# Performance work log

Measured on AMD Instinct MI355X. Metric: run time of the kernel, lower is better.

The kernel has to match this reference:

```python
import jax, jax.numpy as jnp
import numpy as np

N_NODES = 50000
N_EDGES = 800000
IN_C, HID_C, OUT_C = 256, 256, 64


def _glorot(key, shape):
    fan_in, fan_out = shape[1], shape[0]
    lim = float(np.sqrt(6.0 / (fan_in + fan_out)))
    return jax.random.uniform(key, shape, jnp.float32, -lim, lim)


def setup_inputs() -> dict:
    key = jax.random.key(0)
    ks = jax.random.split(key, 8)
    x = jax.random.normal(ks[0], (N_NODES, IN_C), jnp.float32)
    edge_index = jax.random.randint(ks[1], (2, N_EDGES), 0, N_NODES, jnp.int64)
    # layer 1: SAGEConv(IN_C -> HID_C): lin_l (agg neighbors, has bias), lin_r (root, no bias)
    W_l1 = _glorot(ks[2], (HID_C, IN_C))
    b1 = jnp.zeros((HID_C,), jnp.float32)
    W_r1 = _glorot(ks[3], (HID_C, IN_C))
    # layer 2: SAGEConv(HID_C -> OUT_C)
    W_l2 = _glorot(ks[4], (OUT_C, HID_C))
    b2 = jnp.zeros((OUT_C,), jnp.float32)
    W_r2 = _glorot(ks[5], (OUT_C, HID_C))
    return {"x": x, "W_l1": W_l1, "b1": b1, "W_r1": W_r1,
            "W_l2": W_l2, "b2": b2, "W_r2": W_r2, "edge_index": edge_index}


def _sage_conv(x, src, dst, W_l, b, W_r, n_nodes):
    # mean aggregation of source-node features into destination nodes
    msg = x[src]                                               # [E, C]
    agg = jax.ops.segment_sum(msg, dst, num_segments=n_nodes)  # [N, C]
    deg = jax.ops.segment_sum(jnp.ones((src.shape[0],), x.dtype), dst,
                              num_segments=n_nodes)            # [N]
    agg = agg / jnp.maximum(deg, 1.0)[:, None]
    # out = lin_l(agg) + lin_r(x); bias only on lin_l (PyG SAGEConv default)
    return agg @ W_l.T + b + x @ W_r.T


def reference(x, W_l1, b1, W_r1, W_l2, b2, W_r2, edge_index):
    src, dst = edge_index[0], edge_index[1]
    n = x.shape[0]
    h = _sage_conv(x, src, dst, W_l1, b1, W_r1, n)
    h = jax.nn.relu(h)  # dropout is identity in eval mode
    out = _sage_conv(h, src, dst, W_l2, b2, W_r2, n)
    return out
```

## Files before the change

### kernel.cpp

```cpp
#include <hip/hip_runtime.h>

#define IN_C 256
#define HID_C 256
#define OUT_C 64

#define NBK 64
#define NPAD 50176
#define N2 (NPAD / 2)
#define NCH (NPAD / 256)

typedef __attribute__((ext_vector_type(8))) short bf16x8;
typedef __attribute__((ext_vector_type(4))) float f32x4;
typedef __attribute__((ext_vector_type(2))) float f32x2;
typedef __attribute__((ext_vector_type(8))) unsigned short ushortx8;
typedef __attribute__((ext_vector_type(4))) unsigned int u32x4;
typedef __attribute__((ext_vector_type(2))) unsigned int u32x2;

__device__ inline float b2f(unsigned short u) {
    union { unsigned int u; float f; } v; v.u = ((unsigned int)u) << 16; return v.f;
}
__device__ inline unsigned short f2b(float f) {
    union { float f; unsigned int u; } v; v.f = f;
    unsigned int u = v.u;
    unsigned int r = (u + 0x7fffu + ((u >> 16) & 1u)) >> 16;
    return (unsigned short)r;
}

__device__ __forceinline__ unsigned char f2fp8(float v) {
    int pk = __builtin_amdgcn_cvt_pk_fp8_f32(v, v, 0, false);
    return (unsigned char)(pk & 0xff);
}
__device__ __forceinline__ void fp8acc4(unsigned int w, float& a0, float& a1, float& a2, float& a3) {
    f32x2 lo = __builtin_amdgcn_cvt_pk_f32_fp8((int)w, false);
    f32x2 hi = __builtin_amdgcn_cvt_pk_f32_fp8((int)w, true);
    a0 += lo.x; a1 += lo.y; a2 += hi.x; a3 += hi.y;
}

__device__ __forceinline__ void gl2lds16(const ushort* g, ushort* l) {
    __builtin_amdgcn_global_load_lds((const __attribute__((address_space(1))) void*)g,
                                     (__attribute__((address_space(3))) void*)l, 16, 0, 0);
}

__device__ __forceinline__ void conv8(const float* __restrict__ src, ushort* __restrict__ dst, int u) {
    const float4* p = (const float4*)(src + (size_t)u * 8);
    float4 a = p[0], b = p[1];
    ushort4 o0 = make_ushort4(f2b(a.x), f2b(a.y), f2b(a.z), f2b(a.w));
    ushort4 o1 = make_ushort4(f2b(b.x), f2b(b.y), f2b(b.z), f2b(b.w));
    ((ushort4*)(dst + (size_t)u * 8))[0] = o0;
    ((ushort4*)(dst + (size_t)u * 8))[1] = o1;
}


__global__ __launch_bounds__(1024) void k_front(const int* __restrict__ dst, int E, int EPB,
                                                ushort* __restrict__ rank,
                                                unsigned int* __restrict__ cnt32,
                                                int* __restrict__ chunkpart,
                                                const float* __restrict__ x, ushort* __restrict__ xb,
                                                int xUnits,
                                                const float* __restrict__ Wl1, const float* __restrict__ Wr1,
                                                const float* __restrict__ Wl2, const float* __restrict__ Wr2,
                                                ushort* __restrict__ Wc1, ushort* __restrict__ Wc2) {
    const int bid = blockIdx.x;
    const int t = threadIdx.x;

    if (bid < NBK) {
        __shared__ unsigned int h[N2];
        for (int i = t; i < N2; i += 1024) h[i] = 0;
        __syncthreads();

        const int e0 = bid * EPB;
        const int e1 = min(e0 + EPB, E);
        for (int e = e0 + t; e < e1; e += 1024) {
            int d = dst[e];
            int sh = (d & 1) << 4;
            unsigned int old = atomicAdd(&h[d >> 1], 1u << sh);
            rank[e] = (ushort)((old >> sh) & 0xffffu);
        }
        __syncthreads();

        unsigned int* outp = cnt32 + (size_t)bid * N2;
        for (int i = t; i < N2; i += 1024) outp[i] = h[i];

        if (t < NCH) {
            int c = t;
            int sum = 0;
#pragma unroll 8
            for (int j = 0; j < 128; ++j) {
                unsigned int v = h[c * 128 + ((j + c) & 127)];
                sum += (int)(v & 0xffffu) + (int)(v >> 16);
            }
            chunkpart[c * NBK + bid] = sum;
        }
        return;
    }

    const int ct = (bid - NBK) * 1024 + t;
    const int cn = 256 * 1024;
    for (int i = ct; i < 20480; i += cn) {
        if (i < 8192)       conv8(Wl1, Wc1,         i);
        else if (i < 16384) conv8(Wr1, Wc1 + 65536, i - 8192);
        else if (i < 18432) conv8(Wl2, Wc2,         i - 16384);
        else                conv8(Wr2, Wc2 + 16384, i - 18432);
    }
    for (int u = ct; u < xUnits; u += cn) conv8(x, xb, u);
}


__global__ __launch_bounds__(256) void k_scan(const unsigned int* __restrict__ cnt32,
                                              const int* __restrict__ chunkpart, int N,
                                              int* __restrict__ row_start,
                                              ushort* __restrict__ off16) {
    __shared__ int s[256];
    const int bid = blockIdx.x;
    const int t = threadIdx.x;

    int pre = 0;
    const int limit = bid * NBK;
    for (int i = t; i < limit; i += 256) pre += chunkpart[i];
    s[t] = pre;
    __syncthreads();
    for (int o = 128; o > 0; o >>= 1) {
        if (t < o) s[t] += s[t + o];
        __syncthreads();
    }
    const int chunk_off = s[0];
    __syncthreads();

    const int i = bid * 256 + t;
    const ushort* cnt16 = (const ushort*)cnt32;
    int run = 0;
#pragma unroll 8
    for (int b = 0; b < NBK; ++b) {
        ushort cv = cnt16[(size_t)b * NPAD + i];
        off16[(size_t)b * NPAD + i] = (ushort)run;
        run += cv;
    }
    int deg = run;

    s[t] = deg;
    __syncthreads();
    for (int o = 1; o < 256; o <<= 1) {
        int xx = (t >= o) ? s[t - o] : 0;
        __syncthreads();
        s[t] += xx;
        __syncthreads();
    }
    if (i < N) row_start[i + 1] = s[t] + chunk_off;
    if (i == 0) row_start[0] = 0;
}


__global__ __launch_bounds__(256) void k_gemm_mfma(const ushort* __restrict__ A,
                                                   const ushort* __restrict__ W,
                                                   unsigned char* __restrict__ Cp,
                                                   ushort* __restrict__ Cr,
                                                   int N, int K, int PC, int nby, int nwg,
                                                   int nScat,
                                                   const int* __restrict__ src, const int* __restrict__ dst,
                                                   const ushort* __restrict__ rank,
                                                   const int* __restrict__ row_start,
                                                   const ushort* __restrict__ off16,
                                                   int E, int EPB, int* __restrict__ eidx) {
    if (blockIdx.x < (unsigned)nScat) {
        int base = blockIdx.x * 256 + threadIdx.x;
        int stride = nScat * 256;
        for (int e = base; e < E; e += stride) {
            int d = dst[e];
            int b = e / EPB;
            eidx[row_start[d] + (int)off16[(size_t)b * NPAD + d] + (int)rank[e]] = src[e];
        }
        return;
    }

    __shared__ ushort As[128 * 64];
    __shared__ ushort Bs[128 * 64];

    const int orig = blockIdx.x - nScat;
    const int q = nwg >> 3, r = nwg & 7;
    const int xcd = orig & 7;
    const int base = (xcd < r) ? xcd * (q + 1) : r * (q + 1) + (xcd - r) * q;
    const int wgid = base + (orig >> 3);
    const int bx = wgid / nby, by = wgid % nby;

    const int wid  = threadIdx.x >> 6;
    const int lane = threadIdx.x & 63;
    const int wr = wid >> 1, wc = wid & 1;
    const int bm = bx * 128;
    const int bn = by * 128;
    const int lr = lane & 15;
    const int lk = lane >> 4;
    const int srow   = lane >> 3;
    const int schunk = lane & 7;

    f32x4 acc[4][4];
#pragma unroll
    for (int m = 0; m < 4; ++m)
#pragma unroll
        for (int n = 0; n < 4; ++n) acc[m][n] = (f32x4){0.f, 0.f, 0.f, 0.f};

    for (int k0 = 0; k0 < K; k0 += 64) {
#pragma unroll
        for (int i = 0; i < 4; ++i) {
            int seg = wid * 4 + i;
            int row = seg * 8 + srow;
            gl2lds16(A + (size_t)(bm + row) * K + k0 + schunk * 8, As + seg * 512);
            gl2lds16(W + (size_t)(bn + row) * K + k0 + schunk * 8, Bs + seg * 512);
        }
        __syncthreads();

#pragma unroll
        for (int ks = 0; ks < 2; ++ks) {
            bf16x8 a[4], b[4];
#pragma unroll
            for (int m = 0; m < 4; ++m)
                a[m] = *(const bf16x8*)(As + (wr * 64 + m * 16 + lr) * 64 + ks * 32 + lk * 8);
#pragma unroll
            for (int n = 0; n < 4; ++n)
                b[n] = *(const bf16x8*)(Bs + (wc * 64 + n * 16 + lr) * 64 + ks * 32 + lk * 8);
#pragma unroll
            for (int m = 0; m < 4; ++m)
#pragma unroll
                for (int n = 0; n < 4; ++n)
                    acc[m][n] = __builtin_amdgcn_mfma_f32_16x16x32_bf16(a[m], b[n], acc[m][n], 0, 0, 0);
        }
        __syncthreads();
    }

    const bool isP = (bn + wc * 64) < PC;
#pragma unroll
    for (int m = 0; m < 4; ++m)
#pragma unroll
        for (int r2 = 0; r2 < 4; ++r2) {
            int row = bm + wr * 64 + m * 16 + lk * 4 + r2;
            if (row < N) {
                if (isP) {
#pragma unroll
                    for (int n = 0; n < 4; ++n) {
                        int col = bn + wc * 64 + n * 16 + lr;
                        Cp[(size_t)row * PC + col] = f2fp8(acc[m][n][r2]);
                    }
                } else {
#pragma unroll
                    for (int n = 0; n < 4; ++n) {
                        int col = bn + wc * 64 + n * 16 + lr - PC;
                        Cr[(size_t)row * PC + col] = f2b(acc[m][n][r2]);
                    }
                }
            }
        }
}


__global__ __launch_bounds__(256) void k_agg1(const unsigned char* __restrict__ P1,
                                              const ushort* __restrict__ R1,
                                              const float* __restrict__ bias,
                                              const int* __restrict__ row_start,
                                              const int* __restrict__ eidx,
                                              ushort* __restrict__ h, int N) {
    int node = (blockIdx.x * blockDim.x + threadIdx.x) >> 6;
    int lane = threadIdx.x & 63;
    if (node >= N) return;
    const int slot = lane >> 4;
    const int sub  = lane & 15;
    int s0 = row_start[node], s1 = row_start[node + 1];

    float acc[16];
#pragma unroll
    for (int i = 0; i < 16; ++i) acc[i] = 0.f;

    for (int e = s0 + slot; e < s1; e += 16) {
        int e1 = e + 4, e2 = e + 8, e3 = e + 12;
        bool h1 = e1 < s1, h2 = e2 < s1, h3 = e3 < s1;
        int sA = eidx[e];
        int sB = h1 ? eidx[e1] : sA;
        int sC = h2 ? eidx[e2] : sA;
        int sD = h3 ? eidx[e3] : sA;
        u32x4 a = *(const u32x4*)(P1 + (size_t)sA * 256 + sub * 16);
        u32x4 b = *(const u32x4*)(P1 + (size_t)sB * 256 + sub * 16);
        u32x4 c = *(const u32x4*)(P1 + (size_t)sC * 256 + sub * 16);
        u32x4 d = *(const u32x4*)(P1 + (size_t)sD * 256 + sub * 16);
#pragma unroll
        for (int w = 0; w < 4; ++w) fp8acc4(a[w], acc[w*4], acc[w*4+1], acc[w*4+2], acc[w*4+3]);
        if (h1) {
#pragma unroll
            for (int w = 0; w < 4; ++w) fp8acc4(b[w], acc[w*4], acc[w*4+1], acc[w*4+2], acc[w*4+3]);
        }
        if (h2) {
#pragma unroll
            for (int w = 0; w < 4; ++w) fp8acc4(c[w], acc[w*4], acc[w*4+1], acc[w*4+2], acc[w*4+3]);
        }
        if (h3) {
#pragma unroll
            for (int w = 0; w < 4; ++w) fp8acc4(d[w], acc[w*4], acc[w*4+1], acc[w*4+2], acc[w*4+3]);
        }
    }

#pragma unroll
    for (int i = 0; i < 16; ++i) {
        acc[i] += __shfl_xor(acc[i], 16, 64);
        acc[i] += __shfl_xor(acc[i], 32, 64);
    }

    if (slot == 0) {
        int d = s1 - s0;
        float inv = 1.0f / (float)(d > 1 ? d : 1);
        const ushort* rp = R1 + (size_t)node * 256 + sub * 16;
        ushortx8 r0 = *(const ushortx8*)(rp);
        ushortx8 r1 = *(const ushortx8*)(rp + 8);
        const float* bp = bias + sub * 16;
        ushortx8 o0, o1;
#pragma unroll
        for (int i = 0; i < 8; ++i) {
            float v0 = fmaxf(acc[i] * inv + bp[i] + b2f(r0[i]), 0.f);
            float v1 = fmaxf(acc[i + 8] * inv + bp[i + 8] + b2f(r1[i]), 0.f);
            o0[i] = f2b(v0);
            o1[i] = f2b(v1);
        }
        ushort* hp = h + (size_t)node * 256 + sub * 16;
        *(ushortx8*)(hp) = o0;
        *(ushortx8*)(hp + 8) = o1;
    }
}


__global__ __launch_bounds__(256) void k_agg2(const unsigned char* __restrict__ P2,
                                              const ushort* __restrict__ R2,
                                              const float* __restrict__ bias,
                                              const int* __restrict__ row_start,
                                              const int* __restrict__ eidx,
                                              float* __restrict__ out, int N) {
    int node = (blockIdx.x * blockDim.x + threadIdx.x) >> 6;
    int lane = threadIdx.x & 63;
    if (node >= N) return;
    const int slot = lane >> 3;
    const int sub  = lane & 7;
    int s0 = row_start[node], s1 = row_start[node + 1];

    float acc[8];
#pragma unroll
    for (int i = 0; i < 8; ++i) acc[i] = 0.f;

    for (int e = s0 + slot; e < s1; e += 32) {
        int e1 = e + 8, e2 = e + 16, e3 = e + 24;
        bool h1 = e1 < s1, h2 = e2 < s1, h3 = e3 < s1;
        int sA = eidx[e];
        int sB = h1 ? eidx[e1] : sA;
        int sC = h2 ? eidx[e2] : sA;
        int sD = h3 ? eidx[e3] : sA;
        u32x2 a = *(const u32x2*)(P2 + (size_t)sA * 64 + sub * 8);
        u32x2 b = *(const u32x2*)(P2 + (size_t)sB * 64 + sub * 8);
        u32x2 c = *(const u32x2*)(P2 + (size_t)sC * 64 + sub * 8);
        u32x2 d = *(const u32x2*)(P2 + (size_t)sD * 64 + sub * 8);
#pragma unroll
        for (int w = 0; w < 2; ++w) fp8acc4(a[w], acc[w*4], acc[w*4+1], acc[w*4+2], acc[w*4+3]);
        if (h1) {
#pragma unroll
            for (int w = 0; w < 2; ++w) fp8acc4(b[w], acc[w*4], acc[w*4+1], acc[w*4+2], acc[w*4+3]);
        }
        if (h2) {
#pragma unroll
            for (int w = 0; w < 2; ++w) fp8acc4(c[w], acc[w*4], acc[w*4+1], acc[w*4+2], acc[w*4+3]);
        }
        if (h3) {
#pragma unroll
            for (int w = 0; w < 2; ++w) fp8acc4(d[w], acc[w*4], acc[w*4+1], acc[w*4+2], acc[w*4+3]);
        }
    }

#pragma unroll
    for (int i = 0; i < 8; ++i) {
        acc[i] += __shfl_xor(acc[i], 8, 64);
        acc[i] += __shfl_xor(acc[i], 16, 64);
        acc[i] += __shfl_xor(acc[i], 32, 64);
    }

    if (slot == 0) {
        int d = s1 - s0;
        float inv = 1.0f / (float)(d > 1 ? d : 1);
        ushortx8 rv = *(const ushortx8*)(R2 + (size_t)node * 64 + sub * 8);
        const float* bp = bias + sub * 8;
        float o[8];
#pragma unroll
        for (int i = 0; i < 8; ++i) o[i] = acc[i] * inv + bp[i] + b2f(rv[i]);
        float4* op = (float4*)(out + (size_t)node * 64 + sub * 8);
        op[0] = make_float4(o[0], o[1], o[2], o[3]);
        op[1] = make_float4(o[4], o[5], o[6], o[7]);
    }
}


extern "C" void kernel_launch(void* const* d_in, const int* in_sizes, int n_in,
                              void* d_out, int out_size, void* d_ws, size_t ws_size,
                              hipStream_t stream) {
    const float* x    = (const float*)d_in[0];
    const float* W_l1 = (const float*)d_in[1];
    const float* b1   = (const float*)d_in[2];
    const float* W_r1 = (const float*)d_in[3];
    const float* W_l2 = (const float*)d_in[4];
    const float* b2   = (const float*)d_in[5];
    const float* W_r2 = (const float*)d_in[6];
    const int*   ei   = (const int*)d_in[7];

    const int N = in_sizes[0] / IN_C;
    const int E = in_sizes[7] / 2;
    const int EPB = (E + NBK - 1) / NBK;
    const int* src = ei;
    const int* dst = ei + E;

    char* ws = (char*)d_ws;
    size_t off_ = 0;
    auto alloc = [&](size_t bytes) -> void* {
        void* p = ws + off_;
        off_ += (bytes + 255) & ~(size_t)255;
        return p;
    };
    unsigned int*  cnt32     = (unsigned int*)alloc((size_t)NBK * N2 * 4);
    ushort*        off16     = (ushort*)alloc((size_t)NBK * NPAD * 2);
    int*           chunkpart = (int*)alloc((size_t)NCH * NBK * 4);
    int*           row_start = (int*)alloc((size_t)(N + 1) * 4);
    ushort*        rank      = (ushort*)alloc((size_t)E * 2);
    int*           eidx      = (int*)alloc((size_t)E * 4);
    ushort*        xb        = (ushort*)alloc((size_t)N * IN_C * 2);
    ushort*        Wc1       = (ushort*)alloc((size_t)2 * HID_C * IN_C * 2);
    ushort*        Wc2       = (ushort*)alloc((size_t)2 * OUT_C * HID_C * 2);
    unsigned char* P1        = (unsigned char*)alloc((size_t)N * HID_C);
    ushort*        R1        = (ushort*)alloc((size_t)N * HID_C * 2);
    ushort*        h         = (ushort*)alloc((size_t)N * HID_C * 2);
    unsigned char* P2        = (unsigned char*)alloc((size_t)N * OUT_C);
    ushort*        R2        = (ushort*)alloc((size_t)N * OUT_C * 2);
    (void)alloc(128 * 512 * 2);
    (void)ws_size; (void)n_in; (void)out_size;

    {
        int xUnits = N * IN_C / 8;
        k_front<<<NBK + 256, 1024, 0, stream>>>(dst, E, EPB, rank, cnt32, chunkpart,
                                                x, xb, xUnits,
                                                W_l1, W_r1, W_l2, W_r2, Wc1, Wc2);
    }

    k_scan<<<NCH, 256, 0, stream>>>(cnt32, chunkpart, N, row_start, off16);

    {
        const int nScat = 128;
        int nbx = (N + 127) / 128, nby = (2 * HID_C) / 128;
        int nwg = nbx * nby;
        k_gemm_mfma<<<nScat + nwg, 256, 0, stream>>>(xb, Wc1, P1, R1, N, IN_C, HID_C, nby, nwg,
                                                     nScat, src, dst, rank, row_start, off16,
                                                     E, EPB, eidx);
        k_agg1<<<(N + 3) / 4, 256, 0, stream>>>(P1, R1, b1, row_start, eidx, h, N);
    }

    {
        int nbx = (N + 127) / 128, nby = (2 * OUT_C) / 128;
        int nwg = nbx * nby;
        k_gemm_mfma<<<nwg, 256, 0, stream>>>(h, Wc2, P2, R2, N, HID_C, OUT_C, nby, nwg,
                                             0, nullptr, nullptr, nullptr, nullptr, nullptr,
                                             0, 0, nullptr);
        k_agg2<<<(N + 3) / 4, 256, 0, stream>>>(P2, R2, b2, row_start, eidx, (float*)d_out, N);
    }
}
```

Baseline: 149.3 us.

## Replace LDS-tiled GEMM with register-direct double-buffered MFMA kernels per layer

Drops the shared-memory staged 128x128 GEMM and adds two specialized kernels that load bf16 fragments straight from global memory into registers, double-buffered across K steps. Layer 1 uses 32-row tiles with each wave covering 128 output columns, and layer 2 uses 128-row tiles with a single column block. The edge-scatter blocks now work on contiguous edge ranges, and their count rises from 128 to 448. The aim is to remove LDS traffic and barriers and to raise the block count. The cost is redundant global and L2 reads of the weight rows and A rows, plus higher register pressure.

After: 196.4 us. 1.32x slower.

```diff
diff --git a/kernel.cpp b/kernel.cpp
--- a/kernel.cpp
+++ b/kernel.cpp
@@ -34,11 +34,6 @@
     f32x2 lo = __builtin_amdgcn_cvt_pk_f32_fp8((int)w, false);
     f32x2 hi = __builtin_amdgcn_cvt_pk_f32_fp8((int)w, true);
     a0 += lo.x; a1 += lo.y; a2 += hi.x; a3 += hi.y;
-}
-
-__device__ __forceinline__ void gl2lds16(const ushort* g, ushort* l) {
-    __builtin_amdgcn_global_load_lds((const __attribute__((address_space(1))) void*)g,
-                                     (__attribute__((address_space(3))) void*)l, 16, 0, 0);
 }
 
 __device__ __forceinline__ void conv8(const float* __restrict__ src, ushort* __restrict__ dst, int u) {
@@ -150,101 +145,152 @@
 }
 
 
-__global__ __launch_bounds__(256) void k_gemm_mfma(const ushort* __restrict__ A,
-                                                   const ushort* __restrict__ W,
-                                                   unsigned char* __restrict__ Cp,
-                                                   ushort* __restrict__ Cr,
-                                                   int N, int K, int PC, int nby, int nwg,
-                                                   int nScat,
-                                                   const int* __restrict__ src, const int* __restrict__ dst,
-                                                   const ushort* __restrict__ rank,
-                                                   const int* __restrict__ row_start,
-                                                   const ushort* __restrict__ off16,
-                                                   int E, int EPB, int* __restrict__ eidx) {
+__global__ __launch_bounds__(256) void k_gemm_l1(const ushort* __restrict__ A,
+                                                 const ushort* __restrict__ W,
+                                                 unsigned char* __restrict__ Cp,
+                                                 ushort* __restrict__ Cr,
+                                                 int N, int nScat, int nwg,
+                                                 const int* __restrict__ src, const int* __restrict__ dst,
+                                                 const ushort* __restrict__ rank,
+                                                 const int* __restrict__ row_start,
+                                                 const ushort* __restrict__ off16,
+                                                 int E, int EPB, int per, int* __restrict__ eidx) {
     if (blockIdx.x < (unsigned)nScat) {
-        int base = blockIdx.x * 256 + threadIdx.x;
-        int stride = nScat * 256;
-        for (int e = base; e < E; e += stride) {
+        const int e0 = blockIdx.x * per;
+        const int e1 = min(e0 + per, E);
+        for (int e = e0 + (int)threadIdx.x; e < e1; e += 256) {
             int d = dst[e];
             int b = e / EPB;
             eidx[row_start[d] + (int)off16[(size_t)b * NPAD + d] + (int)rank[e]] = src[e];
         }
         return;
     }
-
-    __shared__ ushort As[128 * 64];
-    __shared__ ushort Bs[128 * 64];
 
     const int orig = blockIdx.x - nScat;
     const int q = nwg >> 3, r = nwg & 7;
     const int xcd = orig & 7;
     const int base = (xcd < r) ? xcd * (q + 1) : r * (q + 1) + (xcd - r) * q;
-    const int wgid = base + (orig >> 3);
-    const int bx = wgid / nby, by = wgid % nby;
-
-    const int wid  = threadIdx.x >> 6;
-    const int lane = threadIdx.x & 63;
-    const int wr = wid >> 1, wc = wid & 1;
-    const int bm = bx * 128;
-    const int bn = by * 128;
-    const int lr = lane & 15;
-    const int lk = lane >> 4;
-    const int srow   = lane >> 3;
-    const int schunk = lane & 7;
-
-    f32x4 acc[4][4];
-#pragma unroll
-    for (int m = 0; m < 4; ++m)
-#pragma unroll
-        for (int n = 0; n < 4; ++n) acc[m][n] = (f32x4){0.f, 0.f, 0.f, 0.f};
-
-    for (int k0 = 0; k0 < K; k0 += 64) {
-#pragma unroll
-        for (int i = 0; i < 4; ++i) {
-            int seg = wid * 4 + i;
-            int row = seg * 8 + srow;
-            gl2lds16(A + (size_t)(bm + row) * K + k0 + schunk * 8, As + seg * 512);
-            gl2lds16(W + (size_t)(bn + row) * K + k0 + schunk * 8, Bs + seg * 512);
-        }
-        __syncthreads();
-
-#pragma unroll
-        for (int ks = 0; ks < 2; ++ks) {
-            bf16x8 a[4], b[4];
-#pragma unroll
-            for (int m = 0; m < 4; ++m)
-                a[m] = *(const bf16x8*)(As + (wr * 64 + m * 16 + lr) * 64 + ks * 32 + lk * 8);
-#pragma unroll
-            for (int n = 0; n < 4; ++n)
-                b[n] = *(const bf16x8*)(Bs + (wc * 64 + n * 16 + lr) * 64 + ks * 32 + lk * 8);
-#pragma unroll
-            for (int m = 0; m < 4; ++m)
-#pragma unroll
-                for (int n = 0; n < 4; ++n)
-                    acc[m][n] = __builtin_amdgcn_mfma_f32_16x16x32_bf16(a[m], b[n], acc[m][n], 0, 0, 0);
-        }
-        __syncthreads();
-    }
-
-    const bool isP = (bn + wc * 64) < PC;
-#pragma unroll
-    for (int m = 0; m < 4; ++m)
+    const int bx = base + (orig >> 3);
+
+    const int t = threadIdx.x;
+    const int wid = t >> 6, lane = t & 63;
+    const int lr = lane & 15, lk = lane >> 4;
+    const int rowb = bx * 32;
+    const int colb = wid * 128;
+
+    const ushort* pa0 = A + (size_t)(rowb + lr) * 256 + lk * 8;
+    const ushort* pa1 = pa0 + 16 * 256;
+    const ushort* pb[8];
+#pragma unroll
+    for (int n = 0; n < 8; ++n) pb[n] = W + (size_t)(colb + n * 16 + lr) * 256 + lk * 8;
+
+    f32x4 acc[2][8];
+#pragma unroll
+    for (int m = 0; m < 2; ++m)
+#pragma unroll
+        for (int n = 0; n < 8; ++n) acc[m][n] = (f32x4){0.f, 0.f, 0.f, 0.f};
+
+    bf16x8 aA[2], bA[8], aB[2], bB[8];
+
+#define LD_AB(av, bv, s)                                                   \
+    {                                                                      \
+        av[0] = *(const bf16x8*)(pa0 + (s) * 32);                          \
+        av[1] = *(const bf16x8*)(pa1 + (s) * 32);                          \
+        _Pragma("unroll")                                                  \
+        for (int n_ = 0; n_ < 8; ++n_)                                     \
+            bv[n_] = *(const bf16x8*)(pb[n_] + (s) * 32);                  \
+    }
+#define MM_AB(av, bv)                                                      \
+    {                                                                      \
+        _Pragma("unroll")                                                  \
+        for (int m_ = 0; m_ < 2; ++m_)                                     \
+            _Pragma("unroll")                                              \
+            for (int n_ = 0; n_ < 8; ++n_)                                 \
+                acc[m_][n_] = __builtin_amdgcn_mfma_f32_16x16x32_bf16(     \
+                    av[m_], bv[n_], acc[m_][n_], 0, 0, 0);                 \
+    }
+
+    LD_AB(aA, bA, 0);
+#pragma unroll
+    for (int s = 0; s < 8; s += 2) {
+        if (s + 1 < 8) LD_AB(aB, bB, s + 1);
+        MM_AB(aA, bA);
+        if (s + 2 < 8) LD_AB(aA, bA, s + 2);
+        if (s + 1 < 8) MM_AB(aB, bB);
+    }
+
+    const bool isP = colb < HID_C;
+#pragma unroll
+    for (int m = 0; m < 2; ++m)
 #pragma unroll
         for (int r2 = 0; r2 < 4; ++r2) {
-            int row = bm + wr * 64 + m * 16 + lk * 4 + r2;
+            int row = rowb + m * 16 + lk * 4 + r2;
             if (row < N) {
                 if (isP) {
 #pragma unroll
-                    for (int n = 0; n < 4; ++n) {
-                        int col = bn + wc * 64 + n * 16 + lr;
-                        Cp[(size_t)row * PC + col] = f2fp8(acc[m][n][r2]);
-                    }
+                    for (int n = 0; n < 8; ++n)
+                        Cp[(size_t)row * HID_C + colb + n * 16 + lr] = f2fp8(acc[m][n][r2]);
                 } else {
 #pragma unroll
-                    for (int n = 0; n < 4; ++n) {
-                        int col = bn + wc * 64 + n * 16 + lr - PC;
-                        Cr[(size_t)row * PC + col] = f2b(acc[m][n][r2]);
-                    }
+                    for (int n = 0; n < 8; ++n)
+                        Cr[(size_t)row * HID_C + (colb - HID_C) + n * 16 + lr] = f2b(acc[m][n][r2]);
+                }
+            }
+        }
+}
+
+
+__global__ __launch_bounds__(256) void k_gemm_l2(const ushort* __restrict__ A,
+                                                 const ushort* __restrict__ W,
+                                                 unsigned char* __restrict__ Cp,
+                                                 ushort* __restrict__ Cr,
+                                                 int N, int nwg) {
+    const int orig = blockIdx.x;
+    const int q = nwg >> 3, r = nwg & 7;
+    const int xcd = orig & 7;
+    const int base = (xcd < r) ? xcd * (q + 1) : r * (q + 1) + (xcd - r) * q;
+    const int bx = base + (orig >> 3);
+
+    const int t = threadIdx.x;
+    const int wid = t >> 6, lane = t & 63;
+    const int lr = lane & 15, lk = lane >> 4;
+    const int rowb = bx * 128 + wid * 32;
+
+    const ushort* pa0 = A + (size_t)(rowb + lr) * 256 + lk * 8;
+    const ushort* pa1 = pa0 + 16 * 256;
+    const ushort* pb[8];
+#pragma unroll
+    for (int n = 0; n < 8; ++n) pb[n] = W + (size_t)(n * 16 + lr) * 256 + lk * 8;
+
+    f32x4 acc[2][8];
+#pragma unroll
+    for (int m = 0; m < 2; ++m)
+#pragma unroll
+        for (int n = 0; n < 8; ++n) acc[m][n] = (f32x4){0.f, 0.f, 0.f, 0.f};
+
+    bf16x8 aA[2], bA[8], aB[2], bB[8];
+
+    LD_AB(aA, bA, 0);
+#pragma unroll
+    for (int s = 0; s < 8; s += 2) {
+        if (s + 1 < 8) LD_AB(aB, bB, s + 1);
+        MM_AB(aA, bA);
+        if (s + 2 < 8) LD_AB(aA, bA, s + 2);
+        if (s + 1 < 8) MM_AB(aB, bB);
+    }
+
+#pragma unroll
+    for (int m = 0; m < 2; ++m)
+#pragma unroll
+        for (int r2 = 0; r2 < 4; ++r2) {
+            int row = rowb + m * 16 + lk * 4 + r2;
+            if (row < N) {
+#pragma unroll
+                for (int n = 0; n < 8; ++n) {
+                    if (n < 4)
+                        Cp[(size_t)row * OUT_C + n * 16 + lr] = f2fp8(acc[m][n][r2]);
+                    else
+                        Cr[(size_t)row * OUT_C + (n - 4) * 16 + lr] = f2b(acc[m][n][r2]);
                 }
             }
         }
@@ -441,21 +487,18 @@
     k_scan<<<NCH, 256, 0, stream>>>(cnt32, chunkpart, N, row_start, off16);
 
     {
-        const int nScat = 128;
-        int nbx = (N + 127) / 128, nby = (2 * HID_C) / 128;
-        int nwg = nbx * nby;
-        k_gemm_mfma<<<nScat + nwg, 256, 0, stream>>>(xb, Wc1, P1, R1, N, IN_C, HID_C, nby, nwg,
-                                                     nScat, src, dst, rank, row_start, off16,
-                                                     E, EPB, eidx);
+        const int nScat = 448;
+        const int per = (E + nScat - 1) / nScat;
+        const int nwg = (N + 31) / 32;
+        k_gemm_l1<<<nScat + nwg, 256, 0, stream>>>(xb, Wc1, P1, R1, N, nScat, nwg,
+                                                   src, dst, rank, row_start, off16,
+                                                   E, EPB, per, eidx);
         k_agg1<<<(N + 3) / 4, 256, 0, stream>>>(P1, R1, b1, row_start, eidx, h, N);
     }
 
     {
-        int nbx = (N + 127) / 128, nby = (2 * OUT_C) / 128;
-        int nwg = nbx * nby;
-        k_gemm_mfma<<<nwg, 256, 0, stream>>>(h, Wc2, P2, R2, N, HID_C, OUT_C, nby, nwg,
-                                             0, nullptr, nullptr, nullptr, nullptr, nullptr,
-                                             0, 0, nullptr);
+        const int nwg = (N + 127) / 128;
+        k_gemm_l2<<<nwg, 256, 0, stream>>>(h, Wc2, P2, R2, N, nwg);
         k_agg2<<<(N + 3) / 4, 256, 0, stream>>>(P2, R2, b2, row_start, eidx, (float*)d_out, N);
     }
 }
```
